# Kernel optimization log

Measured on AMD Instinct MI355X. Metric: run time of the kernel, lower is better.

The kernel has to match this reference:

```python
import jax, jax.numpy as jnp
import numpy as np

N_CH = 62
F_DIM = 16
T_DIM = 32
B_DIM = 256
N_NODES = B_DIM * N_CH  # 15872
E_DIM = 200000
SEQ = T_DIM * F_DIM  # 512


def setup_inputs() -> dict:
    key = jax.random.key(0)
    ks = iter(jax.random.split(key, 40))
    s = 0.05
    inp = {}
    inp['x'] = jax.random.normal(next(ks), (N_NODES, F_DIM, T_DIM), dtype=jnp.float32)
    inp['edge_index'] = jax.random.randint(next(ks), (T_DIM, 2, E_DIM), 0, N_NODES, dtype=jnp.int64)
    inp['edge_weight'] = jax.random.uniform(next(ks), (T_DIM, E_DIM), dtype=jnp.float32)
    inp['batch'] = jax.random.randint(next(ks), (T_DIM, N_NODES), 0, B_DIM, dtype=jnp.int64)
    # ChebConv params (K=2): lins have no bias, single bias added at end
    for p in ['c1', 'c2']:
        inp[p + '_w0'] = jax.random.normal(next(ks), (F_DIM, F_DIM), dtype=jnp.float32) * s
        inp[p + '_w1'] = jax.random.normal(next(ks), (F_DIM, F_DIM), dtype=jnp.float32) * s
        inp[p + '_b'] = jnp.zeros((F_DIM,), jnp.float32)
    # LSTM params (torch gate order i,f,g,o); fold b_ih+b_hh into one bias
    for name, i_dim, h_dim in [('l1', N_CH, 64), ('l2', 64, 128), ('l3', 128, 256)]:
        inp[name + '_wih'] = jax.random.normal(next(ks), (4 * h_dim, i_dim), dtype=jnp.float32) * s
        inp[name + '_whh'] = jax.random.normal(next(ks), (4 * h_dim, h_dim), dtype=jnp.float32) * s
        inp[name + '_b'] = jnp.zeros((4 * h_dim,), jnp.float32)
    # MLP head
    for name, i_dim, o_dim in [('fc1', SEQ * 256, 256), ('fc2', 256, 128), ('fc3', 128, 64), ('fc4', 64, 4)]:
        inp[name + '_w'] = jax.random.normal(next(ks), (i_dim, o_dim), dtype=jnp.float32) * s
        inp[name + '_b'] = jnp.zeros((o_dim,), jnp.float32)
    return inp


def _cheb(x, src, dst, w, w0, w1, b):
    # PyG ChebConv K=2, sym norm, lambda_max=2: Tx1 = -D^{-1/2} A D^{-1/2} x
    n = x.shape[0]
    deg = jax.ops.segment_sum(w, src, num_segments=n)
    dinv = jnp.where(deg > 0, jax.lax.rsqrt(deg), 0.0)
    norm = -dinv[src] * w * dinv[dst]
    tx1 = jax.ops.segment_sum(norm[:, None] * x[src], dst, num_segments=n)
    return x @ w0 + tx1 @ w1 + b


def _lstm(x, wih, whh, b):
    # x: [B, S, I] -> [B, S, H], batch_first, zero init state
    bsz, _, _ = x.shape
    h_dim = whh.shape[1]
    xg = x @ wih.T + b  # precompute input gates [B, S, 4H]
    def step(carry, xt):
        h, c = carry
        g = xt + h @ whh.T
        i, f, gg, o = jnp.split(g, 4, axis=-1)
        c = jax.nn.sigmoid(f) * c + jax.nn.sigmoid(i) * jnp.tanh(gg)
        h = jax.nn.sigmoid(o) * jnp.tanh(c)
        return (h, c), h
    h0 = jnp.zeros((bsz, h_dim), x.dtype)
    _, hs = jax.lax.scan(step, (h0, h0), jnp.swapaxes(xg, 0, 1))
    return jnp.swapaxes(hs, 0, 1)


def reference(x, edge_index, edge_weight, batch,
              c1_w0, c1_w1, c1_b, c2_w0, c2_w1, c2_b,
              l1_wih, l1_whh, l1_b, l2_wih, l2_whh, l2_b, l3_wih, l3_whh, l3_b,
              fc1_w, fc1_b, fc2_w, fc2_b, fc3_w, fc3_b, fc4_w, fc4_b):
    def per_t(xt, ei, w):
        h = _cheb(xt, ei[0], ei[1], w, c1_w0, c1_w1, c1_b)
        h = jax.nn.leaky_relu(h, 0.01)
        return _cheb(h, ei[0], ei[1], w, c2_w0, c2_w1, c2_b)
    xt_first = jnp.moveaxis(x, -1, 0)  # [T, N, F]
    h = jax.vmap(per_t)(xt_first, edge_index, edge_weight)  # [T, N, F]
    xc = jnp.moveaxis(h, 0, -1)  # [N, F, T]
    xc = xc.reshape(B_DIM, N_CH, F_DIM, T_DIM)
    xc = jnp.transpose(xc, (0, 3, 2, 1))  # [B, T, F, 62]
    xc = xc.reshape(B_DIM, T_DIM * F_DIM, N_CH)  # [B, S, 62]
    h = _lstm(xc, l1_wih, l1_whh, l1_b)
    h = _lstm(h, l2_wih, l2_whh, l2_b)
    h = _lstm(h, l3_wih, l3_whh, l3_b)
    z = h.reshape(B_DIM, -1)  # [B, S*256]
    z = jax.nn.relu(z @ fc1_w + fc1_b)
    z = jax.nn.relu(z @ fc2_w + fc2_b)
    z = jax.nn.relu(z @ fc3_w + fc3_b)
    return z @ fc4_w + fc4_b
```

## Files before the change

### kernel.cpp

```cpp
#include <hip/hip_runtime.h>
#include <cstdint>
#include <cstddef>


#define T_DIM 32
#define F_DIMC 16
#define NNODE 15872
#define EDGES 200000
#define BATCH 256
#define SEQL 512
#define TN (T_DIM * NNODE)
#define TE (T_DIM * EDGES)

typedef unsigned short ushortT;
typedef __bf16 bf16_t;
typedef bf16_t bf16x8 __attribute__((ext_vector_type(8)));
typedef float f32x4 __attribute__((ext_vector_type(4)));

__device__ __forceinline__ ushortT f2bf(float f) {
  union { float f; unsigned u; } v; v.f = f;
  unsigned u = v.u;
  u += 0x7fffu + ((u >> 16) & 1u);
  return (ushortT)(u >> 16);
}
__device__ __forceinline__ float fsig(float x) { return 1.0f / (1.0f + __expf(-x)); }
__device__ __forceinline__ float ftanh(float x) {
  float e = __expf(2.0f * x);
  return 1.0f - 2.0f / (e + 1.0f);
}
#define PIN(v) asm volatile("" : "+v"(v))

__device__ __forceinline__ void bar_sync() {
  asm volatile("s_waitcnt lgkmcnt(0)\n\ts_barrier" ::: "memory");
  __builtin_amdgcn_sched_barrier(0);
}

__global__ void k_wprep(const float* __restrict__ w1i, const float* __restrict__ w1h,
                        const float* __restrict__ w2i, const float* __restrict__ w2h,
                        const float* __restrict__ w3i, const float* __restrict__ w3h,
                        ushortT* __restrict__ Wcat) {
  int id = blockIdx.x * 256 + threadIdx.x;
  if (id >= 524288) return;
  float v;
  if (id < 32768) {
    int g = id >> 7, k = id & 127;
    v = (k < 62) ? w1i[g * 62 + k] : ((k >= 64) ? w1h[g * 64 + (k - 64)] : 0.0f);
  } else if (id < 131072) {
    int j = id - 32768; int g = j / 192, k = j % 192;
    v = (k < 64) ? w2i[g * 64 + k] : w2h[g * 128 + (k - 64)];
  } else {
    int j = id - 131072; int g = j / 384, k = j % 384;
    v = (k < 128) ? w3i[g * 128 + k] : w3h[g * 256 + (k - 128)];
  }
  Wcat[id] = f2bf(v);
}

__global__ void k_transpose(const float* __restrict__ x, float* __restrict__ xt) {
  __shared__ float s[528];
  int n = blockIdx.x;
  int tid = threadIdx.x;
  for (int i = tid; i < 512; i += 256) {
    s[(i >> 5) * 33 + (i & 31)] = x[(size_t)n * 512 + i];
  }
  __syncthreads();
  for (int i = tid; i < 512; i += 256) {
    int t = i >> 4, f = i & 15;
    xt[((size_t)t * NNODE + n) * 16 + f] = s[f * 33 + t];
  }
}

__global__ void k_degcount(const int* __restrict__ ei, const float* __restrict__ ew,
                           float* __restrict__ deg, int* __restrict__ counts) {
  int id = blockIdx.x * 256 + threadIdx.x;
  if (id >= TE) return;
  int t = id / EDGES, e = id % EDGES;
  int src = ei[(2 * t) * EDGES + e];
  int dst = ei[(2 * t + 1) * EDGES + e];
  atomicAdd(&deg[t * NNODE + src], ew[id]);
  atomicAdd(&counts[t * NNODE + dst], 1);
}

__global__ void k_scanA(const int* __restrict__ counts, int* __restrict__ offs,
                        int* __restrict__ ctot, float* __restrict__ deg) {
  __shared__ int s[256];
  int tid = threadIdx.x;
  int gid = blockIdx.x * 256 + tid;
  float d = deg[gid];
  int v = counts[gid];
  s[tid] = v; __syncthreads();
  for (int off = 1; off < 256; off <<= 1) {
    int x = (tid >= off) ? s[tid - off] : 0;
    __syncthreads();
    s[tid] += x;
    __syncthreads();
  }
  offs[gid] = s[tid] - v;
  if (tid == 255) ctot[blockIdx.x] = s[255];
  deg[gid] = (d > 0.0f) ? rsqrtf(d) : 0.0f;
}

__global__ void k_scanB(const int* __restrict__ ctot, int* __restrict__ cbase) {
  __shared__ int s[256];
  int tid = threadIdx.x;
  int carry = 0;
  for (int c = 0; c < 8; ++c) {
    int i = c * 256 + tid;
    int v = (i < 1984) ? ctot[i] : 0;
    s[tid] = v; __syncthreads();
    for (int off = 1; off < 256; off <<= 1) {
      int x = (tid >= off) ? s[tid - off] : 0;
      __syncthreads();
      s[tid] += x;
      __syncthreads();
    }
    if (i < 1984) cbase[i] = carry + s[tid] - v;
    int tot = s[255];
    __syncthreads();
    carry += tot;
  }
}

__global__ void k_fill(const int* __restrict__ ei, const float* __restrict__ ew,
                       const float* __restrict__ dinv, const int* __restrict__ offs,
                       const int* __restrict__ cbase, int* __restrict__ fillc,
                       int* __restrict__ csrs, float* __restrict__ csrn) {
  int id = blockIdx.x * 256 + threadIdx.x;
  if (id >= TE) return;
  int t = id / EDGES, e = id % EDGES;
  int src = ei[(2 * t) * EDGES + e];
  int dst = ei[(2 * t + 1) * EDGES + e];
  int idx = t * NNODE + dst;
  int pos = offs[idx] + cbase[idx >> 8] + atomicAdd(&fillc[idx], 1);
  csrs[pos] = src;
  csrn[pos] = -dinv[t * NNODE + src] * ew[id] * dinv[idx];
}

__device__ __forceinline__ void fma4(float4& a, float sc, const float4 b) {
  a.x += sc * b.x; a.y += sc * b.y; a.z += sc * b.z; a.w += sc * b.w;
}

__global__ void k_gc(const float* __restrict__ in, const int* __restrict__ offs,
                     const int* __restrict__ cbase,
                     const int* __restrict__ csrs, const float* __restrict__ csrn,
                     const float* __restrict__ w0, const float* __restrict__ w1,
                     const float* __restrict__ bias, float* __restrict__ outF,
                     ushortT* __restrict__ outX, int mode) {
  __shared__ float sw0[256], sw1[256], sb[16];
  int tid = threadIdx.x;
  sw0[tid] = w0[tid];
  sw1[tid] = w1[tid];
  if (tid < 16) sb[tid] = bias[tid];
  __syncthreads();
  int idx = blockIdx.x * 256 + tid;
  if (idx >= TN) return;
  int t = idx / NNODE, n = idx % NNODE;
  const float4* rowp = (const float4*)(in + (size_t)idx * 16);
  float4 x0 = rowp[0], x1 = rowp[1], x2 = rowp[2], x3 = rowp[3];
  float4 a0 = {0, 0, 0, 0}, a1 = {0, 0, 0, 0}, a2 = {0, 0, 0, 0}, a3 = {0, 0, 0, 0};
  int beg = offs[idx] + cbase[idx >> 8];
  int end = (idx == TN - 1) ? TE : offs[idx + 1] + cbase[(idx + 1) >> 8];
  const float* base = in + (size_t)t * NNODE * 16;
  for (int p2 = beg; p2 < end; ++p2) {
    int s = csrs[p2];
    float nr = csrn[p2];
    const float4* rp = (const float4*)(base + (size_t)s * 16);
    fma4(a0, nr, rp[0]); fma4(a1, nr, rp[1]); fma4(a2, nr, rp[2]); fma4(a3, nr, rp[3]);
  }
  float xr[16], ar[16];
  *(float4*)&xr[0] = x0; *(float4*)&xr[4] = x1; *(float4*)&xr[8] = x2; *(float4*)&xr[12] = x3;
  *(float4*)&ar[0] = a0; *(float4*)&ar[4] = a1; *(float4*)&ar[8] = a2; *(float4*)&ar[12] = a3;
  float o[16];
#pragma unroll
  for (int j = 0; j < 16; ++j) o[j] = sb[j];
#pragma unroll
  for (int k = 0; k < 16; ++k) {
    float xv = xr[k], av = ar[k];
#pragma unroll
    for (int j = 0; j < 16; ++j) o[j] += xv * sw0[k * 16 + j] + av * sw1[k * 16 + j];
  }
  if (mode == 0) {
#pragma unroll
    for (int j = 0; j < 16; ++j) o[j] = (o[j] > 0.0f) ? o[j] : 0.01f * o[j];
    float4* op = (float4*)(outF + (size_t)idx * 16);
    op[0] = *(float4*)&o[0]; op[1] = *(float4*)&o[4];
    op[2] = *(float4*)&o[8]; op[3] = *(float4*)&o[12];
  } else {
    int bb = n / 62, ch = n % 62;
#pragma unroll
    for (int j = 0; j < 16; ++j)
      outX[((size_t)(bb * 512 + t * 16 + j)) * 64 + ch] = f2bf(o[j]);
    if (ch < 2) {
#pragma unroll
      for (int j = 0; j < 16; ++j)
        outX[((size_t)(bb * 512 + t * 16 + j)) * 64 + 62 + ch] = 0;
    }
  }
}

__global__ __launch_bounds__(512, 1) void k_lstm(const ushortT* __restrict__ xc,
                                                 const ushortT* __restrict__ Wcat,
                                                 const float* __restrict__ b1g,
                                                 const float* __restrict__ b2g,
                                                 const float* __restrict__ b3g,
                                                 ushortT* __restrict__ zbuf,
                                                 uint32_t* __restrict__ h2x,
                                                 uint32_t* __restrict__ xbuf) {
  __shared__ ushortT X1[2][16 * 72];
  __shared__ ushortT H1[2][16 * 72];
  __shared__ ushortT H2[2][16 * 136];
  __shared__ ushortT HS[2][16 * 136];
  __shared__ ushortT PS[2][16 * 136];
  __shared__ ushortT H2S[2][16 * 136];
  int tid = threadIdx.x;
  int wv = tid >> 6, lane = tid & 63;
  int col = lane & 15, koff = (lane >> 4) * 8, m = lane & 15;
  int bx = blockIdx.x;

  if (bx < 16) {
    int g = bx;
    int bg = g * 16;
    const ushortT* W1 = Wcat;
    const ushortT* W2 = Wcat + 32768;

    bf16x8 w1r[4][4];
    if (wv < 4) {
#pragma unroll
      for (int q = 0; q < 4; ++q)
#pragma unroll
        for (int k = 0; k < 4; ++k) {
          w1r[q][k] = *reinterpret_cast<const bf16x8*>(
              &W1[(size_t)(q * 64 + wv * 16 + col) * 128 + k * 32 + koff]);
          PIN(w1r[q][k]);
        }
    }
    bf16x8 w2r[4][6];
#pragma unroll
    for (int q = 0; q < 4; ++q)
#pragma unroll
      for (int k = 0; k < 6; ++k) {
        w2r[q][k] = *reinterpret_cast<const bf16x8*>(
            &W2[(size_t)(q * 128 + wv * 16 + col) * 192 + k * 32 + koff]);
        PIN(w2r[q][k]);
      }
    float b1v[4] = {0, 0, 0, 0}, b2v[4];
    if (wv < 4) {
#pragma unroll
      for (int q = 0; q < 4; ++q) b1v[q] = b1g[q * 64 + wv * 16 + col];
    }
#pragma unroll
    for (int q = 0; q < 4; ++q) b2v[q] = b2g[q * 128 + wv * 16 + col];

    float c1r[4] = {0, 0, 0, 0};
    float c2r[4] = {0, 0, 0, 0};

    for (int i = tid; i < 2 * 16 * 72; i += 512) { X1[0][i] = 0; H1[0][i] = 0; }
    for (int i = tid; i < 2 * 16 * 136; i += 512) H2[0][i] = 0;
    __syncthreads();
    uint4 xreg = {0, 0, 0, 0};
    {
      int tid2 = tid - 256;
      if (tid2 >= 0 && tid2 < 128) {
        int mm = tid2 >> 3, jj = (tid2 & 7) * 8;
        *(uint4*)&X1[0][mm * 72 + jj] =
            *(const uint4*)&xc[((size_t)(bg + mm) * 512 + 0) * 64 + jj];
        xreg = *(const uint4*)&xc[((size_t)(bg + mm) * 512 + 1) * 64 + jj];
      }
    }
    __syncthreads();

    uint32_t* h2g = h2x + (size_t)g * 512 * 2048;

    for (int t = 0; t < 512; ++t) {
      int pr = t & 1, pw = 1 - pr;
      if (wv < 4) {
        f32x4 acc[4] = {};
#pragma unroll
        for (int kt = 0; kt < 4; ++kt) {
          const ushortT* ap = (kt < 2) ? &X1[pr][m * 72 + kt * 32 + koff]
                                       : &H1[pr][m * 72 + (kt - 2) * 32 + koff];
          bf16x8 a = *reinterpret_cast<const bf16x8*>(ap);
#pragma unroll
          for (int q = 0; q < 4; ++q)
            acc[q] = __builtin_amdgcn_mfma_f32_16x16x32_bf16(a, w1r[q][kt], acc[q], 0, 0, 0);
        }
#pragma unroll
        for (int r = 0; r < 4; ++r) {
          int row = (lane >> 4) * 4 + r;
          int lc = wv * 16 + col;
          float gi = acc[0][r] + b1v[0];
          float gf = acc[1][r] + b1v[1];
          float gg = acc[2][r] + b1v[2];
          float go = acc[3][r] + b1v[3];
          float c = fsig(gf) * c1r[r] + fsig(gi) * ftanh(gg);
          float h = fsig(go) * ftanh(c);
          c1r[r] = c;
          H1[pw][row * 72 + lc] = f2bf(h);
        }
      } else {
        int tid2 = tid - 256;
        if (tid2 < 128) {
          int mm = tid2 >> 3, jj = (tid2 & 7) * 8;
          if (t + 1 < 512)
            *(uint4*)&X1[pw][mm * 72 + jj] = xreg;
          int tf = (t + 2 < 512) ? t + 2 : 511;
          xreg = *(const uint4*)&xc[((size_t)(bg + mm) * 512 + tf) * 64 + jj];
        }
      }
      bar_sync();
      {
        f32x4 acc[4] = {};
#pragma unroll
        for (int kt = 0; kt < 6; ++kt) {
          const ushortT* ap = (kt < 2) ? &H1[pw][m * 72 + kt * 32 + koff]
                                       : &H2[pr][m * 136 + (kt - 2) * 32 + koff];
          bf16x8 a = *reinterpret_cast<const bf16x8*>(ap);
#pragma unroll
          for (int q = 0; q < 4; ++q)
            acc[q] = __builtin_amdgcn_mfma_f32_16x16x32_bf16(a, w2r[q][kt], acc[q], 0, 0, 0);
        }
        uint32_t tag = ((uint32_t)(t + 1)) << 16;
#pragma unroll
        for (int r = 0; r < 4; ++r) {
          int row = (lane >> 4) * 4 + r;
          int lc = wv * 16 + col;
          float gi = acc[0][r] + b2v[0];
          float gf = acc[1][r] + b2v[1];
          float gg = acc[2][r] + b2v[2];
          float go = acc[3][r] + b2v[3];
          float c = fsig(gf) * c2r[r] + fsig(gi) * ftanh(gg);
          float h = fsig(go) * ftanh(c);
          c2r[r] = c;
          ushortT hb = f2bf(h);
          H2[pw][row * 136 + lc] = hb;
          __hip_atomic_store(&h2g[(size_t)t * 2048 + row * 128 + lc], tag | hb,
                             __ATOMIC_RELAXED, __HIP_MEMORY_SCOPE_AGENT);
        }
      }
      bar_sync();
    }
  } else {
    int bxx = bx - 16;
    int s = (bxx >> 3) & 1;
    int g = (bxx & 7) | ((bxx >> 4) << 3);
    int ps = 1 - s;
    int bg = g * 16;
    const ushortT* W3 = Wcat + 131072;

    bf16x8 wH[4][4], wO[4][4], wP[4][4];
#pragma unroll
    for (int q = 0; q < 4; ++q) {
      const ushortT* rw = &W3[(size_t)(q * 256 + s * 128 + wv * 16 + col) * 384];
#pragma unroll
      for (int j = 0; j < 4; ++j) {
        wH[q][j] = *reinterpret_cast<const bf16x8*>(&rw[j * 32 + koff]);
        wO[q][j] = *reinterpret_cast<const bf16x8*>(&rw[(4 + s * 4 + j) * 32 + koff]);
        wP[q][j] = *reinterpret_cast<const bf16x8*>(&rw[(4 + ps * 4 + j) * 32 + koff]);
        PIN(wH[q][j]); PIN(wO[q][j]); PIN(wP[q][j]);
      }
    }
    float b3v[4];
#pragma unroll
    for (int q = 0; q < 4; ++q) b3v[q] = b3g[q * 256 + s * 128 + wv * 16 + col];

    float c3r[4] = {0, 0, 0, 0};

    for (int i = tid; i < 2 * 16 * 136; i += 512) HS[0][i] = 0;
    __syncthreads();

    uint32_t* myslot = xbuf + (((size_t)g * 2 + s) * 2) * 2048;
    const uint32_t* pslot = xbuf + (((size_t)g * 2 + ps) * 2) * 2048;
    const uint32_t* h2g = h2x + (size_t)g * 512 * 2048;

    int prow = tid >> 5, pc0 = (tid & 31) * 4;

    {
      const uint32_t* hp = h2g + prow * 128 + pc0;
      uint32_t u0 = __hip_atomic_load(hp + 0, __ATOMIC_RELAXED, __HIP_MEMORY_SCOPE_AGENT);
      uint32_t u1 = __hip_atomic_load(hp + 1, __ATOMIC_RELAXED, __HIP_MEMORY_SCOPE_AGENT);
      uint32_t u2 = __hip_atomic_load(hp + 2, __ATOMIC_RELAXED, __HIP_MEMORY_SCOPE_AGENT);
      uint32_t u3 = __hip_atomic_load(hp + 3, __ATOMIC_RELAXED, __HIP_MEMORY_SCOPE_AGENT);
      for (;;) {
        bool ok = ((u0 >> 16) == 1u) & ((u1 >> 16) == 1u) &
                  ((u2 >> 16) == 1u) & ((u3 >> 16) == 1u);
        if (ok) break;
        u0 = __hip_atomic_load(hp + 0, __ATOMIC_RELAXED, __HIP_MEMORY_SCOPE_AGENT);
        u1 = __hip_atomic_load(hp + 1, __ATOMIC_RELAXED, __HIP_MEMORY_SCOPE_AGENT);
        u2 = __hip_atomic_load(hp + 2, __ATOMIC_RELAXED, __HIP_MEMORY_SCOPE_AGENT);
        u3 = __hip_atomic_load(hp + 3, __ATOMIC_RELAXED, __HIP_MEMORY_SCOPE_AGENT);
      }
      H2S[0][prow * 136 + pc0 + 0] = (ushortT)(u0 & 0xffffu);
      H2S[0][prow * 136 + pc0 + 1] = (ushortT)(u1 & 0xffffu);
      H2S[0][prow * 136 + pc0 + 2] = (ushortT)(u2 & 0xffffu);
      H2S[0][prow * 136 + pc0 + 3] = (ushortT)(u3 & 0xffffu);
    }
    __syncthreads();

    for (int t = 0; t < 512; ++t) {
      int prt = t & 1, pw = 1 - prt;
      const uint32_t* pb = pslot + (size_t)prt * 2048 + prow * 128 + pc0;
      uint32_t v0 = 0, v1 = 0, v2 = 0, v3 = 0;
      if (t > 0) {
        v0 = __hip_atomic_load(pb + 0, __ATOMIC_RELAXED, __HIP_MEMORY_SCOPE_AGENT);
        v1 = __hip_atomic_load(pb + 1, __ATOMIC_RELAXED, __HIP_MEMORY_SCOPE_AGENT);
        v2 = __hip_atomic_load(pb + 2, __ATOMIC_RELAXED, __HIP_MEMORY_SCOPE_AGENT);
        v3 = __hip_atomic_load(pb + 3, __ATOMIC_RELAXED, __HIP_MEMORY_SCOPE_AGENT);
      }
      const uint32_t* hp = h2g + (size_t)(t + 1) * 2048 + prow * 128 + pc0;
      uint32_t u0 = 0, u1 = 0, u2 = 0, u3 = 0;
      if (t < 511) {
        u0 = __hip_atomic_load(hp + 0, __ATOMIC_RELAXED, __HIP_MEMORY_SCOPE_AGENT);
        u1 = __hip_atomic_load(hp + 1, __ATOMIC_RELAXED, __HIP_MEMORY_SCOPE_AGENT);
        u2 = __hip_atomic_load(hp + 2, __ATOMIC_RELAXED, __HIP_MEMORY_SCOPE_AGENT);
        u3 = __hip_atomic_load(hp + 3, __ATOMIC_RELAXED, __HIP_MEMORY_SCOPE_AGENT);
      }
      __builtin_amdgcn_sched_barrier(0);
      f32x4 acc[4] = {};
#pragma unroll
      for (int kt = 0; kt < 4; ++kt) {
        bf16x8 a = *reinterpret_cast<const bf16x8*>(&H2S[prt][m * 136 + kt * 32 + koff]);
#pragma unroll
        for (int q = 0; q < 4; ++q)
          acc[q] = __builtin_amdgcn_mfma_f32_16x16x32_bf16(a, wH[q][kt], acc[q], 0, 0, 0);
      }
      if (t > 0) {
#pragma unroll
        for (int j = 0; j < 4; ++j) {
          bf16x8 a = *reinterpret_cast<const bf16x8*>(&HS[prt][m * 136 + j * 32 + koff]);
#pragma unroll
          for (int q = 0; q < 4; ++q)
            acc[q] = __builtin_amdgcn_mfma_f32_16x16x32_bf16(a, wO[q][j], acc[q], 0, 0, 0);
        }
        {
          uint32_t want = (uint32_t)t;
          while (((v0 >> 16) != want) | ((v1 >> 16) != want) |
                 ((v2 >> 16) != want) | ((v3 >> 16) != want)) {
            v0 = __hip_atomic_load(pb + 0, __ATOMIC_RELAXED, __HIP_MEMORY_SCOPE_AGENT);
            v1 = __hip_atomic_load(pb + 1, __ATOMIC_RELAXED, __HIP_MEMORY_SCOPE_AGENT);
            v2 = __hip_atomic_load(pb + 2, __ATOMIC_RELAXED, __HIP_MEMORY_SCOPE_AGENT);
            v3 = __hip_atomic_load(pb + 3, __ATOMIC_RELAXED, __HIP_MEMORY_SCOPE_AGENT);
          }
          PS[prt][prow * 136 + pc0 + 0] = (ushortT)(v0 & 0xffffu);
          PS[prt][prow * 136 + pc0 + 1] = (ushortT)(v1 & 0xffffu);
          PS[prt][prow * 136 + pc0 + 2] = (ushortT)(v2 & 0xffffu);
          PS[prt][prow * 136 + pc0 + 3] = (ushortT)(v3 & 0xffffu);
        }
        bar_sync();
#pragma unroll
        for (int j = 0; j < 4; ++j) {
          bf16x8 a = *reinterpret_cast<const bf16x8*>(&PS[prt][m * 136 + j * 32 + koff]);
#pragma unroll
          for (int q = 0; q < 4; ++q)
            acc[q] = __builtin_amdgcn_mfma_f32_16x16x32_bf16(a, wP[q][j], acc[q], 0, 0, 0);
        }
      }
      if (t < 511) {
        uint32_t want = (uint32_t)(t + 2);
        while (((u0 >> 16) != want) | ((u1 >> 16) != want) |
               ((u2 >> 16) != want) | ((u3 >> 16) != want)) {
          u0 = __hip_atomic_load(hp + 0, __ATOMIC_RELAXED, __HIP_MEMORY_SCOPE_AGENT);
          u1 = __hip_atomic_load(hp + 1, __ATOMIC_RELAXED, __HIP_MEMORY_SCOPE_AGENT);
          u2 = __hip_atomic_load(hp + 2, __ATOMIC_RELAXED, __HIP_MEMORY_SCOPE_AGENT);
          u3 = __hip_atomic_load(hp + 3, __ATOMIC_RELAXED, __HIP_MEMORY_SCOPE_AGENT);
        }
        H2S[pw][prow * 136 + pc0 + 0] = (ushortT)(u0 & 0xffffu);
        H2S[pw][prow * 136 + pc0 + 1] = (ushortT)(u1 & 0xffffu);
        H2S[pw][prow * 136 + pc0 + 2] = (ushortT)(u2 & 0xffffu);
        H2S[pw][prow * 136 + pc0 + 3] = (ushortT)(u3 & 0xffffu);
      }
      uint32_t* mw = myslot + (size_t)((t + 1) & 1) * 2048;
      ushortT hbs[4];
#pragma unroll
      for (int r = 0; r < 4; ++r) {
        int row = (lane >> 4) * 4 + r;
        int lc = wv * 16 + col;
        float gi = acc[0][r] + b3v[0];
        float gf = acc[1][r] + b3v[1];
        float gg = acc[2][r] + b3v[2];
        float go = acc[3][r] + b3v[3];
        float c = fsig(gf) * c3r[r] + fsig(gi) * ftanh(gg);
        float h = fsig(go) * ftanh(c);
        c3r[r] = c;
        hbs[r] = f2bf(h);
        __hip_atomic_store(mw + row * 128 + lc, ((uint32_t)(t + 1) << 16) | hbs[r],
                           __ATOMIC_RELAXED, __HIP_MEMORY_SCOPE_AGENT);
      }
      asm volatile("s_waitcnt vmcnt(0)" ::: "memory");
      __builtin_amdgcn_sched_barrier(0);
#pragma unroll
      for (int r = 0; r < 4; ++r) {
        int row = (lane >> 4) * 4 + r;
        int lc = wv * 16 + col;
        HS[pw][row * 136 + lc] = hbs[r];
        zbuf[((size_t)(bg + row) * 512 + t) * 256 + s * 128 + lc] = hbs[r];
      }
      bar_sync();
    }
  }
}

__global__ __launch_bounds__(256) void k_fc1(const ushortT* __restrict__ zbuf,
                                             const float* __restrict__ w,
                                             float* __restrict__ part) {
  __shared__ ushortT As[256 * 40];
  __shared__ ushortT Bs[64 * 40];
  int tid = threadIdx.x;
  int kb = blockIdx.x;
  int nb = blockIdx.y;
  int wv = tid >> 6, lane = tid & 63;
  int col = lane & 15, koff = (lane >> 4) * 8;
  int k0base = kb * 2048;
  f32x4 acc[4][4] = {};
  for (int kt = 0; kt < 64; ++kt) {
    int k0 = k0base + kt * 32;
    {
      const uint4* src = (const uint4*)(zbuf + (size_t)tid * 131072 + k0);
// ... 74 lines not shown
  const float* c2w1 = (const float*)d_in[8];
  const float* c2b  = (const float*)d_in[9];
  const float* l1wi = (const float*)d_in[10];
  const float* l1wh = (const float*)d_in[11];
  const float* l1b  = (const float*)d_in[12];
  const float* l2wi = (const float*)d_in[13];
  const float* l2wh = (const float*)d_in[14];
  const float* l2b  = (const float*)d_in[15];
  const float* l3wi = (const float*)d_in[16];
  const float* l3wh = (const float*)d_in[17];
  const float* l3b  = (const float*)d_in[18];
  const float* fc1w = (const float*)d_in[19];
  const float* fc1b = (const float*)d_in[20];
  const float* fc2w = (const float*)d_in[21];
  const float* fc2b = (const float*)d_in[22];
  const float* fc3w = (const float*)d_in[23];
  const float* fc3b = (const float*)d_in[24];
  const float* fc4w = (const float*)d_in[25];
  const float* fc4b = (const float*)d_in[26];
  float* out = (float*)d_out;

  char* p = (char*)d_ws;
  auto alloc = [&](size_t bytes) { void* r = (void*)p; p += (bytes + 255) & ~(size_t)255; return r; };
  float* xt      = (float*)alloc(32505856);
  float* h1buf   = (float*)alloc(32505856);
  float* dinv    = (float*)alloc(2031616);
  int* counts    = (int*)alloc(2031616);
  int* offs      = (int*)alloc(2031616);
  int* fillc     = (int*)alloc(2031616);
  int* ctot      = (int*)alloc(8192);
  int* cbase     = (int*)alloc(8192);
  int* csrs      = (int*)alloc(25600000);
  float* csrn    = (float*)alloc(25600000);
  ushortT* xc    = (ushortT*)alloc(16777216);
  ushortT* Wcat  = (ushortT*)alloc(1048576);
  ushortT* zbuf  = (ushortT*)alloc(67108864);
  float* part    = (float*)alloc(16777216);
  float* fo1     = (float*)alloc(262144);
  float* fo2     = (float*)alloc(131072);
  float* fo3     = (float*)alloc(65536);
  uint32_t* xbuf = (uint32_t*)alloc(524288);
  uint32_t* h2x = (uint32_t*)xt;

  hipMemsetAsync(dinv, 0, 2031616, stream);
  hipMemsetAsync(counts, 0, 2031616, stream);
  hipMemsetAsync(fillc, 0, 2031616, stream);

  k_wprep<<<2048, 256, 0, stream>>>(l1wi, l1wh, l2wi, l2wh, l3wi, l3wh, Wcat);
  k_transpose<<<15872, 256, 0, stream>>>(x, xt);
  k_degcount<<<25000, 256, 0, stream>>>(ei, ew, dinv, counts);
  k_scanA<<<1984, 256, 0, stream>>>(counts, offs, ctot, dinv);
  k_scanB<<<1, 256, 0, stream>>>(ctot, cbase);
  k_fill<<<25000, 256, 0, stream>>>(ei, ew, dinv, offs, cbase, fillc, csrs, csrn);
  k_gc<<<1984, 256, 0, stream>>>(xt, offs, cbase, csrs, csrn, c1w0, c1w1, c1b, h1buf, nullptr, 0);
  k_gc<<<1984, 256, 0, stream>>>(h1buf, offs, cbase, csrs, csrn, c2w0, c2w1, c2b, nullptr, xc, 1);
  hipMemsetAsync(h2x, 0, 67108864, stream);
  k_lstm<<<48, 512, 0, stream>>>(xc, Wcat, l1b, l2b, l3b, zbuf, h2x, xbuf);
  k_fc1<<<dim3(64, 4), 256, 0, stream>>>(zbuf, fc1w, part);
  k_fc1red<<<64, 256, 0, stream>>>(part, fc1b, fo1);
  k_fcv<<<128, 256, 0, stream>>>(fo1, fc2w, fc2b, fo2, 256, 128, 1);
  k_fcv<<<64, 256, 0, stream>>>(fo2, fc3w, fc3b, fo3, 128, 64, 1);
  k_fcv<<<4, 256, 0, stream>>>(fo3, fc4w, fc4b, out, 64, 4, 0);
}
```

Baseline: 3.606 ms.

## Fuse graph conv into LSTM kernel with per-timestep producer blocks and tagged handoff

The CSR build (degree, scan, fill) and both ChebConv layers move into 32 extra blocks of the LSTM kernel, one per timestep, doing everything in shared memory. They publish bf16 outputs into a 32-bit buffer tagged with the timestep, and LSTM layer-1 blocks spin on those tags, so the recurrence can start while later timesteps are still being convolved. This removes six kernel launches and the global-atomic CSR build. The cost is that each timestep's graph work now runs on a single block, a doubled-size xc buffer, and spin-waits that need all 80 blocks to be co-resident.

```diff
diff --git a/kernel.cpp b/kernel.cpp
--- a/kernel.cpp
+++ b/kernel.cpp
@@ -33,6 +33,13 @@
 __device__ __forceinline__ void bar_sync() {
   asm volatile("s_waitcnt lgkmcnt(0)\n\ts_barrier" ::: "memory");
   __builtin_amdgcn_sched_barrier(0);
+}
+
+__device__ __forceinline__ uint32_t aload(const uint32_t* p) {
+  return __hip_atomic_load(p, __ATOMIC_RELAXED, __HIP_MEMORY_SCOPE_AGENT);
+}
+__device__ __forceinline__ void astore(uint32_t* p, uint32_t v) {
+  __hip_atomic_store(p, v, __ATOMIC_RELAXED, __HIP_MEMORY_SCOPE_AGENT);
 }
 
 __global__ void k_wprep(const float* __restrict__ w1i, const float* __restrict__ w1h,
@@ -69,154 +76,163 @@
   }
 }
 
-__global__ void k_degcount(const int* __restrict__ ei, const float* __restrict__ ew,
-                           float* __restrict__ deg, int* __restrict__ counts) {
-  int id = blockIdx.x * 256 + threadIdx.x;
-  if (id >= TE) return;
-  int t = id / EDGES, e = id % EDGES;
-  int src = ei[(2 * t) * EDGES + e];
-  int dst = ei[(2 * t + 1) * EDGES + e];
-  atomicAdd(&deg[t * NNODE + src], ew[id]);
-  atomicAdd(&counts[t * NNODE + dst], 1);
-}
-
-__global__ void k_scanA(const int* __restrict__ counts, int* __restrict__ offs,
-                        int* __restrict__ ctot, float* __restrict__ deg) {
-  __shared__ int s[256];
-  int tid = threadIdx.x;
-  int gid = blockIdx.x * 256 + tid;
-  float d = deg[gid];
-  int v = counts[gid];
-  s[tid] = v; __syncthreads();
-  for (int off = 1; off < 256; off <<= 1) {
-    int x = (tid >= off) ? s[tid - off] : 0;
-    __syncthreads();
-    s[tid] += x;
-    __syncthreads();
-  }
-  offs[gid] = s[tid] - v;
-  if (tid == 255) ctot[blockIdx.x] = s[255];
-  deg[gid] = (d > 0.0f) ? rsqrtf(d) : 0.0f;
-}
-
-__global__ void k_scanB(const int* __restrict__ ctot, int* __restrict__ cbase) {
-  __shared__ int s[256];
-  int tid = threadIdx.x;
-  int carry = 0;
-  for (int c = 0; c < 8; ++c) {
-    int i = c * 256 + tid;
-    int v = (i < 1984) ? ctot[i] : 0;
-    s[tid] = v; __syncthreads();
-    for (int off = 1; off < 256; off <<= 1) {
-      int x = (tid >= off) ? s[tid - off] : 0;
-      __syncthreads();
-      s[tid] += x;
-      __syncthreads();
-    }
-    if (i < 1984) cbase[i] = carry + s[tid] - v;
-    int tot = s[255];
-    __syncthreads();
-    carry += tot;
-  }
-}
-
-__global__ void k_fill(const int* __restrict__ ei, const float* __restrict__ ew,
-                       const float* __restrict__ dinv, const int* __restrict__ offs,
-                       const int* __restrict__ cbase, int* __restrict__ fillc,
-                       int* __restrict__ csrs, float* __restrict__ csrn) {
-  int id = blockIdx.x * 256 + threadIdx.x;
-  if (id >= TE) return;
-  int t = id / EDGES, e = id % EDGES;
-  int src = ei[(2 * t) * EDGES + e];
-  int dst = ei[(2 * t + 1) * EDGES + e];
-  int idx = t * NNODE + dst;
-  int pos = offs[idx] + cbase[idx >> 8] + atomicAdd(&fillc[idx], 1);
-  csrs[pos] = src;
-  csrn[pos] = -dinv[t * NNODE + src] * ew[id] * dinv[idx];
-}
-
 __device__ __forceinline__ void fma4(float4& a, float sc, const float4 b) {
   a.x += sc * b.x; a.y += sc * b.y; a.z += sc * b.z; a.w += sc * b.w;
 }
 
-__global__ void k_gc(const float* __restrict__ in, const int* __restrict__ offs,
-                     const int* __restrict__ cbase,
-                     const int* __restrict__ csrs, const float* __restrict__ csrn,
-                     const float* __restrict__ w0, const float* __restrict__ w1,
-                     const float* __restrict__ bias, float* __restrict__ outF,
-                     ushortT* __restrict__ outX, int mode) {
-  __shared__ float sw0[256], sw1[256], sb[16];
-  int tid = threadIdx.x;
-  sw0[tid] = w0[tid];
-  sw1[tid] = w1[tid];
-  if (tid < 16) sb[tid] = bias[tid];
-  __syncthreads();
-  int idx = blockIdx.x * 256 + tid;
-  if (idx >= TN) return;
-  int t = idx / NNODE, n = idx % NNODE;
-  const float4* rowp = (const float4*)(in + (size_t)idx * 16);
-  float4 x0 = rowp[0], x1 = rowp[1], x2 = rowp[2], x3 = rowp[3];
-  float4 a0 = {0, 0, 0, 0}, a1 = {0, 0, 0, 0}, a2 = {0, 0, 0, 0}, a3 = {0, 0, 0, 0};
-  int beg = offs[idx] + cbase[idx >> 8];
-  int end = (idx == TN - 1) ? TE : offs[idx + 1] + cbase[(idx + 1) >> 8];
-  const float* base = in + (size_t)t * NNODE * 16;
-  for (int p2 = beg; p2 < end; ++p2) {
-    int s = csrs[p2];
-    float nr = csrn[p2];
-    const float4* rp = (const float4*)(base + (size_t)s * 16);
-    fma4(a0, nr, rp[0]); fma4(a1, nr, rp[1]); fma4(a2, nr, rp[2]); fma4(a3, nr, rp[3]);
-  }
-  float xr[16], ar[16];
-  *(float4*)&xr[0] = x0; *(float4*)&xr[4] = x1; *(float4*)&xr[8] = x2; *(float4*)&xr[12] = x3;
-  *(float4*)&ar[0] = a0; *(float4*)&ar[4] = a1; *(float4*)&ar[8] = a2; *(float4*)&ar[12] = a3;
-  float o[16];
-#pragma unroll
-  for (int j = 0; j < 16; ++j) o[j] = sb[j];
-#pragma unroll
-  for (int k = 0; k < 16; ++k) {
-    float xv = xr[k], av = ar[k];
-#pragma unroll
-    for (int j = 0; j < 16; ++j) o[j] += xv * sw0[k * 16 + j] + av * sw1[k * 16 + j];
-  }
-  if (mode == 0) {
-#pragma unroll
-    for (int j = 0; j < 16; ++j) o[j] = (o[j] > 0.0f) ? o[j] : 0.01f * o[j];
-    float4* op = (float4*)(outF + (size_t)idx * 16);
-    op[0] = *(float4*)&o[0]; op[1] = *(float4*)&o[4];
-    op[2] = *(float4*)&o[8]; op[3] = *(float4*)&o[12];
-  } else {
-    int bb = n / 62, ch = n % 62;
-#pragma unroll
-    for (int j = 0; j < 16; ++j)
-      outX[((size_t)(bb * 512 + t * 16 + j)) * 64 + ch] = f2bf(o[j]);
-    if (ch < 2) {
-#pragma unroll
-      for (int j = 0; j < 16; ++j)
-        outX[((size_t)(bb * 512 + t * 16 + j)) * 64 + 62 + ch] = 0;
-    }
-  }
-}
-
-__global__ __launch_bounds__(512, 1) void k_lstm(const ushortT* __restrict__ xc,
-                                                 const ushortT* __restrict__ Wcat,
-                                                 const float* __restrict__ b1g,
-                                                 const float* __restrict__ b2g,
-                                                 const float* __restrict__ b3g,
-                                                 ushortT* __restrict__ zbuf,
-                                                 uint32_t* __restrict__ h2x,
-                                                 uint32_t* __restrict__ xbuf) {
-  __shared__ ushortT X1[2][16 * 72];
-  __shared__ ushortT H1[2][16 * 72];
-  __shared__ ushortT H2[2][16 * 136];
-  __shared__ ushortT HS[2][16 * 136];
-  __shared__ ushortT PS[2][16 * 136];
-  __shared__ ushortT H2S[2][16 * 136];
+__global__ __launch_bounds__(512, 1) void k_lstm(
+    const float* __restrict__ xt, const int* __restrict__ ei,
+    const float* __restrict__ ew,
+    const float* __restrict__ c1w0, const float* __restrict__ c1w1,
+    const float* __restrict__ c1b,
+    const float* __restrict__ c2w0, const float* __restrict__ c2w1,
+    const float* __restrict__ c2b,
+    const ushortT* __restrict__ Wcat,
+    const float* __restrict__ b1g, const float* __restrict__ b2g,
+    const float* __restrict__ b3g,
+    int* __restrict__ csrs, float* __restrict__ csrn,
+    float* __restrict__ h1buf, uint32_t* __restrict__ xc32,
+    ushortT* __restrict__ zbuf, uint32_t* __restrict__ h2x,
+    uint32_t* __restrict__ xbuf) {
+  __shared__ __align__(16) unsigned char smem[131136];
   int tid = threadIdx.x;
   int wv = tid >> 6, lane = tid & 63;
   int col = lane & 15, koff = (lane >> 4) * 8, m = lane & 15;
   int bx = blockIdx.x;
 
+  if (bx >= 48) {
+    int t = bx - 48;
+    float* sdeg = (float*)smem;
+    int* soffs = (int*)(smem + 63488);
+    int* spart = (int*)(smem + 126976);
+    float* swa = (float*)(smem + 129024);
+    float* swb = (float*)(smem + 130048);
+    float* sbb = (float*)(smem + 131072);
+    const int* srcp = ei + (size_t)(2 * t) * EDGES;
+    const int* dstp = ei + (size_t)(2 * t + 1) * EDGES;
+    const float* ewp = ew + (size_t)t * EDGES;
+    int* csrsp = csrs + (size_t)t * EDGES;
+    float* csrnp = csrn + (size_t)t * EDGES;
+    for (int i = tid; i < NNODE; i += 512) { sdeg[i] = 0.0f; soffs[i] = 0; }
+    __syncthreads();
+    for (int e = tid; e < EDGES; e += 512) {
+      atomicAdd(&sdeg[srcp[e]], ewp[e]);
+      atomicAdd(&soffs[dstp[e]], 1);
+    }
+    __syncthreads();
+    for (int i = tid; i < NNODE; i += 512) {
+      float d = sdeg[i];
+      sdeg[i] = (d > 0.0f) ? rsqrtf(d) : 0.0f;
+    }
+    {
+      int base = tid * 31, sum = 0;
+#pragma unroll
+      for (int j = 0; j < 31; ++j) { int v = soffs[base + j]; soffs[base + j] = sum; sum += v; }
+      spart[tid] = sum;
+    }
+    __syncthreads();
+    for (int off = 1; off < 512; off <<= 1) {
+      int xv = (tid >= off) ? spart[tid - off] : 0;
+      __syncthreads();
+      spart[tid] += xv;
+      __syncthreads();
+    }
+    {
+      int add = (tid == 0) ? 0 : spart[tid - 1];
+      int base = tid * 31;
+#pragma unroll
+      for (int j = 0; j < 31; ++j) soffs[base + j] += add;
+    }
+    __syncthreads();
+    for (int e = tid; e < EDGES; e += 512) {
+      int src = srcp[e], dst = dstp[e];
+      float w = ewp[e];
+      int pos = atomicAdd(&soffs[dst], 1);
+      csrsp[pos] = src;
+      csrnp[pos] = -sdeg[src] * w * sdeg[dst];
+    }
+    __syncthreads();
+    if (tid < 256) { swa[tid] = c1w0[tid]; swb[tid] = c1w1[tid]; }
+    if (tid < 16) sbb[tid] = c1b[tid];
+    __syncthreads();
+    const float* xtt = xt + (size_t)t * NNODE * 16;
+    float* h1t = h1buf + (size_t)t * NNODE * 16;
+    for (int n = tid; n < NNODE; n += 512) {
+      int beg = (n == 0) ? 0 : soffs[n - 1];
+      int end = soffs[n];
+      const float4* rowp = (const float4*)(xtt + (size_t)n * 16);
+      float4 x0 = rowp[0], x1 = rowp[1], x2 = rowp[2], x3 = rowp[3];
+      float4 a0 = {0, 0, 0, 0}, a1 = {0, 0, 0, 0}, a2 = {0, 0, 0, 0}, a3 = {0, 0, 0, 0};
+      for (int p2 = beg; p2 < end; ++p2) {
+        int s = csrsp[p2];
+        float nr = csrnp[p2];
+        const float4* rp = (const float4*)(xtt + (size_t)s * 16);
+        fma4(a0, nr, rp[0]); fma4(a1, nr, rp[1]); fma4(a2, nr, rp[2]); fma4(a3, nr, rp[3]);
+      }
+      float xr[16], ar[16];
+      *(float4*)&xr[0] = x0; *(float4*)&xr[4] = x1; *(float4*)&xr[8] = x2; *(float4*)&xr[12] = x3;
+      *(float4*)&ar[0] = a0; *(float4*)&ar[4] = a1; *(float4*)&ar[8] = a2; *(float4*)&ar[12] = a3;
+      float o[16];
+#pragma unroll
+      for (int j = 0; j < 16; ++j) o[j] = sbb[j];
+#pragma unroll
+      for (int k = 0; k < 16; ++k) {
+        float xv = xr[k], av = ar[k];
+#pragma unroll
+        for (int j = 0; j < 16; ++j) o[j] += xv * swa[k * 16 + j] + av * swb[k * 16 + j];
+      }
+      float4* op = (float4*)(h1t + (size_t)n * 16);
+#pragma unroll
+      for (int j = 0; j < 16; ++j) o[j] = (o[j] > 0.0f) ? o[j] : 0.01f * o[j];
+      op[0] = *(float4*)&o[0]; op[1] = *(float4*)&o[4];
+      op[2] = *(float4*)&o[8]; op[3] = *(float4*)&o[12];
+    }
+    __syncthreads();
+    if (tid < 256) { swa[tid] = c2w0[tid]; swb[tid] = c2w1[tid]; }
+    if (tid < 16) sbb[tid] = c2b[tid];
+    __syncthreads();
+    uint32_t tag = ((uint32_t)(t + 1)) << 16;
+    for (int n = tid; n < NNODE; n += 512) {
+      int beg = (n == 0) ? 0 : soffs[n - 1];
+      int end = soffs[n];
+      const float4* rowp = (const float4*)(h1t + (size_t)n * 16);
+      float4 x0 = rowp[0], x1 = rowp[1], x2 = rowp[2], x3 = rowp[3];
+      float4 a0 = {0, 0, 0, 0}, a1 = {0, 0, 0, 0}, a2 = {0, 0, 0, 0}, a3 = {0, 0, 0, 0};
+      for (int p2 = beg; p2 < end; ++p2) {
+        int s = csrsp[p2];
+        float nr = csrnp[p2];
+        const float4* rp = (const float4*)(h1t + (size_t)s * 16);
+        fma4(a0, nr, rp[0]); fma4(a1, nr, rp[1]); fma4(a2, nr, rp[2]); fma4(a3, nr, rp[3]);
+      }
+      float xr[16], ar[16];
+      *(float4*)&xr[0] = x0; *(float4*)&xr[4] = x1; *(float4*)&xr[8] = x2; *(float4*)&xr[12] = x3;
+      *(float4*)&ar[0] = a0; *(float4*)&ar[4] = a1; *(float4*)&ar[8] = a2; *(float4*)&ar[12] = a3;
+      float o[16];
+#pragma unroll
+      for (int j = 0; j < 16; ++j) o[j] = sbb[j];
+#pragma unroll
+      for (int k = 0; k < 16; ++k) {
+        float xv = xr[k], av = ar[k];
+#pragma unroll
+        for (int j = 0; j < 16; ++j) o[j] += xv * swa[k * 16 + j] + av * swb[k * 16 + j];
+      }
+      int bb = n / 62, ch = n % 62;
+#pragma unroll
+      for (int j = 0; j < 16; ++j)
+        astore(&xc32[((size_t)(bb * 512 + t * 16 + j)) * 64 + ch], tag | f2bf(o[j]));
+      if (ch < 2) {
+#pragma unroll
+        for (int j = 0; j < 16; ++j)
+          astore(&xc32[((size_t)(bb * 512 + t * 16 + j)) * 64 + 62 + ch], tag);
+      }
+    }
+    return;
+  }
+
   if (bx < 16) {
+    ushortT* X1f = (ushortT*)smem;
+    ushortT* H1f = (ushortT*)(smem + 4608);
+    ushortT* H2f = (ushortT*)(smem + 9216);
     int g = bx;
     int bg = g * 16;
     const ushortT* W1 = Wcat;
@@ -253,17 +269,45 @@
     float c1r[4] = {0, 0, 0, 0};
     float c2r[4] = {0, 0, 0, 0};
 
-    for (int i = tid; i < 2 * 16 * 72; i += 512) { X1[0][i] = 0; H1[0][i] = 0; }
-    for (int i = tid; i < 2 * 16 * 136; i += 512) H2[0][i] = 0;
+    for (int i = tid; i < 2 * 16 * 72; i += 512) { X1f[i] = 0; H1f[i] = 0; }
+    for (int i = tid; i < 2 * 16 * 136; i += 512) H2f[i] = 0;
     __syncthreads();
     uint4 xreg = {0, 0, 0, 0};
     {
       int tid2 = tid - 256;
       if (tid2 >= 0 && tid2 < 128) {
         int mm = tid2 >> 3, jj = (tid2 & 7) * 8;
-        *(uint4*)&X1[0][mm * 72 + jj] =
-            *(const uint4*)&xc[((size_t)(bg + mm) * 512 + 0) * 64 + jj];
-        xreg = *(const uint4*)&xc[((size_t)(bg + mm) * 512 + 1) * 64 + jj];
+        const uint32_t* p0 = &xc32[((size_t)(bg + mm) * 512 + 0) * 64 + jj];
+        uint32_t w[8];
+#pragma unroll
+        for (int i = 0; i < 8; ++i) w[i] = aload(p0 + i);
+        for (;;) {
+          bool ok = true;
+#pragma unroll
+          for (int i = 0; i < 8; ++i)
+            if ((w[i] >> 16) != 1u) { ok = false; w[i] = aload(p0 + i); }
+          if (ok) break;
+        }
+        uint4 v;
+        v.x = (w[0] & 0xffffu) | (w[1] << 16);
+        v.y = (w[2] & 0xffffu) | (w[3] << 16);
+        v.z = (w[4] & 0xffffu) | (w[5] << 16);
+        v.w = (w[6] & 0xffffu) | (w[7] << 16);
+        *(uint4*)&X1f[mm * 72 + jj] = v;
+        const uint32_t* p1 = &xc32[((size_t)(bg + mm) * 512 + 1) * 64 + jj];
+#pragma unroll
+        for (int i = 0; i < 8; ++i) w[i] = aload(p1 + i);
+        for (;;) {
+          bool ok = true;
+#pragma unroll
+          for (int i = 0; i < 8; ++i)
+            if ((w[i] >> 16) != 1u) { ok = false; w[i] = aload(p1 + i); }
+          if (ok) break;
+        }
+        xreg.x = (w[0] & 0xffffu) | (w[1] << 16);
+        xreg.y = (w[2] & 0xffffu) | (w[3] << 16);
+        xreg.z = (w[4] & 0xffffu) | (w[5] << 16);
+        xreg.w = (w[6] & 0xffffu) | (w[7] << 16);
       }
     }
     __syncthreads();
@@ -276,8 +320,8 @@
         f32x4 acc[4] = {};
 #pragma unroll
         for (int kt = 0; kt < 4; ++kt) {
-          const ushortT* ap = (kt < 2) ? &X1[pr][m * 72 + kt * 32 + koff]
-                                       : &H1[pr][m * 72 + (kt - 2) * 32 + koff];
+          const ushortT* ap = (kt < 2) ? &X1f[pr * 1152 + m * 72 + kt * 32 + koff]
+                                       : &H1f[pr * 1152 + m * 72 + (kt - 2) * 32 + koff];
           bf16x8 a = *reinterpret_cast<const bf16x8*>(ap);
 #pragma unroll
           for (int q = 0; q < 4; ++q)
@@ -294,16 +338,31 @@
           float c = fsig(gf) * c1r[r] + fsig(gi) * ftanh(gg);
           float h = fsig(go) * ftanh(c);
           c1r[r] = c;
-          H1[pw][row * 72 + lc] = f2bf(h);
+          H1f[pw * 1152 + row * 72 + lc] = f2bf(h);
         }
       } else {
         int tid2 = tid - 256;
         if (tid2 < 128) {
           int mm = tid2 >> 3, jj = (tid2 & 7) * 8;
           if (t + 1 < 512)
-            *(uint4*)&X1[pw][mm * 72 + jj] = xreg;
+            *(uint4*)&X1f[pw * 1152 + mm * 72 + jj] = xreg;
           int tf = (t + 2 < 512) ? t + 2 : 511;
-          xreg = *(const uint4*)&xc[((size_t)(bg + mm) * 512 + tf) * 64 + jj];
+          const uint32_t* pp = &xc32[((size_t)(bg + mm) * 512 + tf) * 64 + jj];
+          uint32_t want = (uint32_t)((tf >> 4) + 1);
+          uint32_t w[8];
+#pragma unroll
+          for (int i = 0; i < 8; ++i) w[i] = aload(pp + i);
+          for (;;) {
+            bool ok = true;
+#pragma unroll
+            for (int i = 0; i < 8; ++i)
+              if ((w[i] >> 16) != want) { ok = false; w[i] = aload(pp + i); }
+            if (ok) break;
+          }
+          xreg.x = (w[0] & 0xffffu) | (w[1] << 16);
+          xreg.y = (w[2] & 0xffffu) | (w[3] << 16);
+          xreg.z = (w[4] & 0xffffu) | (w[5] << 16);
+          xreg.w = (w[6] & 0xffffu) | (w[7] << 16);
         }
       }
       bar_sync();
@@ -311,8 +370,8 @@
         f32x4 acc[4] = {};
 #pragma unroll
         for (int kt = 0; kt < 6; ++kt) {
-          const ushortT* ap = (kt < 2) ? &H1[pw][m * 72 + kt * 32 + koff]
-                                       : &H2[pr][m * 136 + (kt - 2) * 32 + koff];
+          const ushortT* ap = (kt < 2) ? &H1f[pw * 1152 + m * 72 + kt * 32 + koff]
+                                       : &H2f[pr * 2176 + m * 136 + (kt - 2) * 32 + koff];
           bf16x8 a = *reinterpret_cast<const bf16x8*>(ap);
 #pragma unroll
           for (int q = 0; q < 4; ++q)
@@ -331,14 +390,16 @@
           float h = fsig(go) * ftanh(c);
           c2r[r] = c;
           ushortT hb = f2bf(h);
-          H2[pw][row * 136 + lc] = hb;
-          __hip_atomic_store(&h2g[(size_t)t * 2048 + row * 128 + lc], tag | hb,
-                             __ATOMIC_RELAXED, __HIP_MEMORY_SCOPE_AGENT);
+          H2f[pw * 2176 + row * 136 + lc] = hb;
+          astore(&h2g[(size_t)t * 2048 + row * 128 + lc], tag | hb);
         }
       }
       bar_sync();
     }
   } else {
+    ushortT* HSf = (ushortT*)smem;
+    ushortT* PSf = (ushortT*)(smem + 8704);
+    ushortT* H2Sf = (ushortT*)(smem + 17408);
     int bxx = bx - 16;
     int s = (bxx >> 3) & 1;
     int g = (bxx & 7) | ((bxx >> 4) << 3);
@@ -364,7 +425,7 @@
 
     float c3r[4] = {0, 0, 0, 0};
 
-    for (int i = tid; i < 2 * 16 * 136; i += 512) HS[0][i] = 0;
+    for (int i = tid; i < 2 * 16 * 136; i += 512) HSf[i] = 0;
     __syncthreads();
 
     uint32_t* myslot = xbuf + (((size_t)g * 2 + s) * 2) * 2048;
@@ -375,23 +436,17 @@
 
     {
       const uint32_t* hp = h2g + prow * 128 + pc0;
-      uint32_t u0 = __hip_atomic_load(hp + 0, __ATOMIC_RELAXED, __HIP_MEMORY_SCOPE_AGENT);
-      uint32_t u1 = __hip_atomic_load(hp + 1, __ATOMIC_RELAXED, __HIP_MEMORY_SCOPE_AGENT);
-      uint32_t u2 = __hip_atomic_load(hp + 2, __ATOMIC_RELAXED, __HIP_MEMORY_SCOPE_AGENT);
-      uint32_t u3 = __hip_atomic_load(hp + 3, __ATOMIC_RELAXED, __HIP_MEMORY_SCOPE_AGENT);
+      uint32_t u0 = aload(hp + 0), u1 = aload(hp + 1), u2 = aload(hp + 2), u3 = aload(hp + 3);
       for (;;) {
         bool ok = ((u0 >> 16) == 1u) & ((u1 >> 16) == 1u) &
                   ((u2 >> 16) == 1u) & ((u3 >> 16) == 1u);
         if (ok) break;
-        u0 = __hip_atomic_load(hp + 0, __ATOMIC_RELAXED, __HIP_MEMORY_SCOPE_AGENT);
-        u1 = __hip_atomic_load(hp + 1, __ATOMIC_RELAXED, __HIP_MEMORY_SCOPE_AGENT);
-        u2 = __hip_atomic_load(hp + 2, __ATOMIC_RELAXED, __HIP_MEMORY_SCOPE_AGENT);
-        u3 = __hip_atomic_load(hp + 3, __ATOMIC_RELAXED, __HIP_MEMORY_SCOPE_AGENT);
-      }
-      H2S[0][prow * 136 + pc0 + 0] = (ushortT)(u0 & 0xffffu);
-      H2S[0][prow * 136 + pc0 + 1] = (ushortT)(u1 & 0xffffu);
-      H2S[0][prow * 136 + pc0 + 2] = (ushortT)(u2 & 0xffffu);
-      H2S[0][prow * 136 + pc0 + 3] = (ushortT)(u3 & 0xffffu);
+        u0 = aload(hp + 0); u1 = aload(hp + 1); u2 = aload(hp + 2); u3 = aload(hp + 3);
+      }
+      H2Sf[prow * 136 + pc0 + 0] = (ushortT)(u0 & 0xffffu);
+      H2Sf[prow * 136 + pc0 + 1] = (ushortT)(u1 & 0xffffu);
+      H2Sf[prow * 136 + pc0 + 2] = (ushortT)(u2 & 0xffffu);
+      H2Sf[prow * 136 + pc0 + 3] = (ushortT)(u3 & 0xffffu);
     }
     __syncthreads();
 
@@ -400,24 +455,18 @@
       const uint32_t* pb = pslot + (size_t)prt * 2048 + prow * 128 + pc0;
       uint32_t v0 = 0, v1 = 0, v2 = 0, v3 = 0;
       if (t > 0) {
-        v0 = __hip_atomic_load(pb + 0, __ATOMIC_RELAXED, __HIP_MEMORY_SCOPE_AGENT);
-        v1 = __hip_atomic_load(pb + 1, __ATOMIC_RELAXED, __HIP_MEMORY_SCOPE_AGENT);
-        v2 = __hip_atomic_load(pb + 2, __ATOMIC_RELAXED, __HIP_MEMORY_SCOPE_AGENT);
-        v3 = __hip_atomic_load(pb + 3, __ATOMIC_RELAXED, __HIP_MEMORY_SCOPE_AGENT);
+        v0 = aload(pb + 0); v1 = aload(pb + 1); v2 = aload(pb + 2); v3 = aload(pb + 3);
       }
       const uint32_t* hp = h2g + (size_t)(t + 1) * 2048 + prow * 128 + pc0;
       uint32_t u0 = 0, u1 = 0, u2 = 0, u3 = 0;
       if (t < 511) {
-        u0 = __hip_atomic_load(hp + 0, __ATOMIC_RELAXED, __HIP_MEMORY_SCOPE_AGENT);
-        u1 = __hip_atomic_load(hp + 1, __ATOMIC_RELAXED, __HIP_MEMORY_SCOPE_AGENT);
-        u2 = __hip_atomic_load(hp + 2, __ATOMIC_RELAXED, __HIP_MEMORY_SCOPE_AGENT);
-        u3 = __hip_atomic_load(hp + 3, __ATOMIC_RELAXED, __HIP_MEMORY_SCOPE_AGENT);
+        u0 = aload(hp + 0); u1 = aload(hp + 1); u2 = aload(hp + 2); u3 = aload(hp + 3);
       }
       __builtin_amdgcn_sched_barrier(0);
       f32x4 acc[4] = {};
 #pragma unroll
       for (int kt = 0; kt < 4; ++kt) {
-        bf16x8 a = *reinterpret_cast<const bf16x8*>(&H2S[prt][m * 136 + kt * 32 + koff]);
+        bf16x8 a = *reinterpret_cast<const bf16x8*>(&H2Sf[prt * 2176 + m * 136 + kt * 32 + koff]);
 #pragma unroll
         for (int q = 0; q < 4; ++q)
           acc[q] = __builtin_amdgcn_mfma_f32_16x16x32_bf16(a, wH[q][kt], acc[q], 0, 0, 0);
@@ -425,7 +474,7 @@
       if (t > 0) {
 #pragma unroll
         for (int j = 0; j < 4; ++j) {
-          bf16x8 a = *reinterpret_cast<const bf16x8*>(&HS[prt][m * 136 + j * 32 + koff]);
+          bf16x8 a = *reinterpret_cast<const bf16x8*>(&HSf[prt * 2176 + m * 136 + j * 32 + koff]);
 #pragma unroll
           for (int q = 0; q < 4; ++q)
             acc[q] = __builtin_amdgcn_mfma_f32_16x16x32_bf16(a, wO[q][j], acc[q], 0, 0, 0);
@@ -434,20 +483,17 @@
           uint32_t want = (uint32_t)t;
           while (((v0 >> 16) != want) | ((v1 >> 16) != want) |
                  ((v2 >> 16) != want) | ((v3 >> 16) != want)) {
-            v0 = __hip_atomic_load(pb + 0, __ATOMIC_RELAXED, __HIP_MEMORY_SCOPE_AGENT);
-            v1 = __hip_atomic_load(pb + 1, __ATOMIC_RELAXED, __HIP_MEMORY_SCOPE_AGENT);
-            v2 = __hip_atomic_load(pb + 2, __ATOMIC_RELAXED, __HIP_MEMORY_SCOPE_AGENT);
-            v3 = __hip_atomic_load(pb + 3, __ATOMIC_RELAXED, __HIP_MEMORY_SCOPE_AGENT);
+            v0 = aload(pb + 0); v1 = aload(pb + 1); v2 = aload(pb + 2); v3 = aload(pb + 3);
           }
-          PS[prt][prow * 136 + pc0 + 0] = (ushortT)(v0 & 0xffffu);
-          PS[prt][prow * 136 + pc0 + 1] = (ushortT)(v1 & 0xffffu);
-          PS[prt][prow * 136 + pc0 + 2] = (ushortT)(v2 & 0xffffu);
-          PS[prt][prow * 136 + pc0 + 3] = (ushortT)(v3 & 0xffffu);
+          PSf[prt * 2176 + prow * 136 + pc0 + 0] = (ushortT)(v0 & 0xffffu);
+          PSf[prt * 2176 + prow * 136 + pc0 + 1] = (ushortT)(v1 & 0xffffu);
+          PSf[prt * 2176 + prow * 136 + pc0 + 2] = (ushortT)(v2 & 0xffffu);
+          PSf[prt * 2176 + prow * 136 + pc0 + 3] = (ushortT)(v3 & 0xffffu);
         }
         bar_sync();
 #pragma unroll
         for (int j = 0; j < 4; ++j) {
-          bf16x8 a = *reinterpret_cast<const bf16x8*>(&PS[prt][m * 136 + j * 32 + koff]);
+          bf16x8 a = *reinterpret_cast<const bf16x8*>(&PSf[prt * 2176 + m * 136 + j * 32 + koff]);
 #pragma unroll
           for (int q = 0; q < 4; ++q)
             acc[q] = __builtin_amdgcn_mfma_f32_16x16x32_bf16(a, wP[q][j], acc[q], 0, 0, 0);
@@ -457,15 +503,12 @@
         uint32_t want = (uint32_t)(t + 2);
         while (((u0 >> 16) != want) | ((u1 >> 16) != want) |
                ((u2 >> 16) != want) | ((u3 >> 16) != want)) {
-          u0 = __hip_atomic_load(hp + 0, __ATOMIC_RELAXED, __HIP_MEMORY_SCOPE_AGENT);
-          u1 = __hip_atomic_load(hp + 1, __ATOMIC_RELAXED, __HIP_MEMORY_SCOPE_AGENT);
-          u2 = __hip_atomic_load(hp + 2, __ATOMIC_RELAXED, __HIP_MEMORY_SCOPE_AGENT);
-          u3 = __hip_atomic_load(hp + 3, __ATOMIC_RELAXED, __HIP_MEMORY_SCOPE_AGENT);
-        }
-        H2S[pw][prow * 136 + pc0 + 0] = (ushortT)(u0 & 0xffffu);
-        H2S[pw][prow * 136 + pc0 + 1] = (ushortT)(u1 & 0xffffu);
-        H2S[pw][prow * 136 + pc0 + 2] = (ushortT)(u2 & 0xffffu);
-        H2S[pw][prow * 136 + pc0 + 3] = (ushortT)(u3 & 0xffffu);
+          u0 = aload(hp + 0); u1 = aload(hp + 1); u2 = aload(hp + 2); u3 = aload(hp + 3);
+        }
+        H2Sf[pw * 2176 + prow * 136 + pc0 + 0] = (ushortT)(u0 & 0xffffu);
+        H2Sf[pw * 2176 + prow * 136 + pc0 + 1] = (ushortT)(u1 & 0xffffu);
+        H2Sf[pw * 2176 + prow * 136 + pc0 + 2] = (ushortT)(u2 & 0xffffu);
+        H2Sf[pw * 2176 + prow * 136 + pc0 + 3] = (ushortT)(u3 & 0xffffu);
       }
       uint32_t* mw = myslot + (size_t)((t + 1) & 1) * 2048;
       ushortT hbs[4];
@@ -481,8 +524,7 @@
         float h = fsig(go) * ftanh(c);
         c3r[r] = c;
         hbs[r] = f2bf(h);
-        __hip_atomic_store(mw + row * 128 + lc, ((uint32_t)(t + 1) << 16) | hbs[r],
-                           __ATOMIC_RELAXED, __HIP_MEMORY_SCOPE_AGENT);
+        astore(mw + row * 128 + lc, ((uint32_t)(t + 1) << 16) | hbs[r]);
       }
       asm volatile("s_waitcnt vmcnt(0)" ::: "memory");
       __builtin_amdgcn_sched_barrier(0);
@@ -490,7 +532,7 @@
       for (int r = 0; r < 4; ++r) {
         int row = (lane >> 4) * 4 + r;
         int lc = wv * 16 + col;
-        HS[pw][row * 136 + lc] = hbs[r];
+        HSf[pw * 2176 + row * 136 + lc] = hbs[r];
         zbuf[((size_t)(bg + row) * 512 + t) * 256 + s * 128 + lc] = hbs[r];
       }
       bar_sync();
@@ -611,40 +653,29 @@
 
   char* p = (char*)d_ws;
   auto alloc = [&](size_t bytes) { void* r = (void*)p; p += (bytes + 255) & ~(size_t)255; return r; };
-  float* xt      = (float*)alloc(32505856);
-  float* h1buf   = (float*)alloc(32505856);
-  float* dinv    = (float*)alloc(2031616);
-  int* counts    = (int*)alloc(2031616);
-  int* offs      = (int*)alloc(2031616);
-  int* fillc     = (int*)alloc(2031616);
-  int* ctot      = (int*)alloc(8192);
-  int* cbase     = (int*)alloc(8192);
-  int* csrs      = (int*)alloc(25600000);
-  float* csrn    = (float*)alloc(25600000);
-  ushortT* xc    = (ushortT*)alloc(16777216);
-  ushortT* Wcat  = (ushortT*)alloc(1048576);
-  ushortT* zbuf  = (ushortT*)alloc(67108864);
-  float* part    = (float*)alloc(16777216);
-  float* fo1     = (float*)alloc(262144);
-  float* fo2     = (float*)alloc(131072);
-  float* fo3     = (float*)alloc(65536);
-  uint32_t* xbuf = (uint32_t*)alloc(524288);
-  uint32_t* h2x = (uint32_t*)xt;
-
-  hipMemsetAsync(dinv, 0, 2031616, stream);
-  hipMemsetAsync(counts, 0, 2031616, stream);
-  hipMemsetAsync(fillc, 0, 2031616, stream);
+  float* xt        = (float*)alloc(32505856);
+  float* h1buf     = (float*)alloc(32505856);
+  int* csrs        = (int*)alloc(25600000);
+  float* csrn      = (float*)alloc(25600000);
+  uint32_t* xc32   = (uint32_t*)alloc(134217728 / 4);
+  ushortT* Wcat    = (ushortT*)alloc(1048576);
+  ushortT* zbuf    = (ushortT*)alloc(67108864);
+  char* scratch    = (char*)alloc(67108864);
+  uint32_t* xbuf   = (uint32_t*)alloc(524288);
+  uint32_t* h2x = (uint32_t*)scratch;
+  float* part = (float*)scratch;
+  float* fo1 = (float*)(scratch + 16777216);
+  float* fo2 = (float*)(scratch + 16777216 + 262144);
+  float* fo3 = (float*)(scratch + 16777216 + 262144 + 131072);
+
+  hipMemsetAsync(h2x, 0, 67108864, stream);
+  hipMemsetAsync(xc32, 0, 33554432, stream);
 
   k_wprep<<<2048, 256, 0, stream>>>(l1wi, l1wh, l2wi, l2wh, l3wi, l3wh, Wcat);
   k_transpose<<<15872, 256, 0, stream>>>(x, xt);
-  k_degcount<<<25000, 256, 0, stream>>>(ei, ew, dinv, counts);
-  k_scanA<<<1984, 256, 0, stream>>>(counts, offs, ctot, dinv);
-  k_scanB<<<1, 256, 0, stream>>>(ctot, cbase);
-  k_fill<<<25000, 256, 0, stream>>>(ei, ew, dinv, offs, cbase, fillc, csrs, csrn);
-  k_gc<<<1984, 256, 0, stream>>>(xt, offs, cbase, csrs, csrn, c1w0, c1w1, c1b, h1buf, nullptr, 0);
-  k_gc<<<1984, 256, 0, stream>>>(h1buf, offs, cbase, csrs, csrn, c2w0, c2w1, c2b, nullptr, xc, 1);
-  hipMemsetAsync(h2x, 0, 67108864, stream);
-  k_lstm<<<48, 512, 0, stream>>>(xc, Wcat, l1b, l2b, l3b, zbuf, h2x, xbuf);
+  k_lstm<<<80, 512, 0, stream>>>(xt, ei, ew, c1w0, c1w1, c1b, c2w0, c2w1, c2b,
+                                 Wcat, l1b, l2b, l3b, csrs, csrn, h1buf, xc32,
+                                 zbuf, h2x, xbuf);
   k_fc1<<<dim3(64, 4), 256, 0, stream>>>(zbuf, fc1w, part);
   k_fc1red<<<64, 256, 0, stream>>>(part, fc1b, fo1);
   k_fcv<<<128, 256, 0, stream>>>(fo1, fc2w, fc2b, fo2, 256, 128, 1);
```

Result: slower. 5.083 ms (+40.9%).
